# Performance work log

Hardware: AMD Instinct MI355X
Metric: run time of the kernel (lower is better)

Reference implementation:

```python
import jax, jax.numpy as jnp
import numpy as np

N_ATOMS = 100000
N_MOLS = 2500
MAX_NB = 10
HID = 256
ATOM_FDIM = 151
FEAT_DIM = 200
FFN_HID = 1024
N_TASKS = 12
LN_EPS = 1e-5


def setup_inputs() -> dict:
    key = jax.random.key(0)
    ks = jax.random.split(key, 12)
    atoms_per_mol = N_ATOMS // N_MOLS  # 40
    starts = jnp.arange(N_MOLS, dtype=jnp.int32) * atoms_per_mol
    sizes = jnp.full((N_MOLS,), atoms_per_mol, dtype=jnp.int32)
    a_scope = jnp.stack([starts, sizes], axis=1)  # [M, 2]
    d_in = HID + ATOM_FDIM  # 407
    d_ff = 4 * HID          # 1024
    d_mol_in = HID + FEAT_DIM  # 456
    def lin(k, fan_in, shape):
        return jax.random.uniform(k, shape, jnp.float32, -1.0, 1.0) / np.sqrt(fan_in)
    return {
        "atom_output": jax.random.normal(ks[0], (N_ATOMS, HID), jnp.float32),
        "original_f_atoms": jax.random.uniform(ks[1], (N_ATOMS, ATOM_FDIM), jnp.float32),
        "a2a": jax.random.randint(ks[2], (N_ATOMS, MAX_NB), 0, N_ATOMS, jnp.int32),
        "a_scope": a_scope,
        "features_batch": jax.random.normal(ks[3], (N_MOLS, FEAT_DIM), jnp.float32),
        "W1": lin(ks[4], d_in, (d_in, d_ff)), "b1": jnp.zeros((d_ff,), jnp.float32),
        "W2": lin(ks[5], d_ff, (d_ff, HID)), "b2": jnp.zeros((HID,), jnp.float32),
        "ln_g": jnp.ones((HID,), jnp.float32), "ln_b": jnp.zeros((HID,), jnp.float32),
        "Wm1": lin(ks[6], d_mol_in, (d_mol_in, FFN_HID)), "bm1": jnp.zeros((FFN_HID,), jnp.float32),
        "Wm2": lin(ks[7], FFN_HID, (FFN_HID, N_TASKS)), "bm2": jnp.zeros((N_TASKS,), jnp.float32),
    }


def reference(atom_output, original_f_atoms, a2a, a_scope, features_batch,
              W1, b1, W2, b2, ln_g, ln_b, Wm1, bm1, Wm2, bm2):
    # select_neighbor_and_aggregate: gather neighbor embeddings and sum
    aggr = atom_output[a2a].sum(axis=1)                      # [N, HID]
    x = jnp.concatenate([original_f_atoms, aggr], axis=1)    # [N, HID+ATOM_FDIM]
    # PositionwiseFeedForward (dropout = identity at eval)
    h = jax.nn.relu(x @ W1 + b1) @ W2 + b2                   # [N, HID]
    # SublayerConnection with x=None: LayerNorm (dropout identity)
    mu = h.mean(axis=-1, keepdims=True)
    var = ((h - mu) ** 2).mean(axis=-1, keepdims=True)
    h = (h - mu) * jax.lax.rsqrt(var + LN_EPS) * ln_g + ln_b
    # Readout: mean over variable-length a_scope ranges (segment mean)
    starts = a_scope[:, 0]
    sizes = a_scope[:, 1]
    n_mols = a_scope.shape[0]
    seg_ids = jnp.searchsorted(starts, jnp.arange(h.shape[0], dtype=starts.dtype), side="right") - 1
    sums = jax.ops.segment_sum(h, seg_ids, num_segments=n_mols)   # [M, HID]
    mol = sums / sizes[:, None].astype(h.dtype)
    # concat molecule-level features, then mol FFN (2 layers)
    mol = jnp.concatenate([mol, features_batch], axis=1)          # [M, HID+FEAT_DIM]
    out = jax.nn.relu(mol @ Wm1 + bm1) @ Wm2 + bm2                # [M, N_TASKS]
    return out
```

## Files before the change

### kernel.cpp

```cpp
#include <hip/hip_runtime.h>

typedef __attribute__((ext_vector_type(8))) short bfrag;
typedef __attribute__((ext_vector_type(4))) float f32x4;

__device__ __forceinline__ float bf2f(unsigned short u) {
    union { unsigned u32; float f; } cv; cv.u32 = ((unsigned)u) << 16; return cv.f;
}
__device__ __forceinline__ unsigned short f2bf(float f) {
    union { float f; unsigned u; } cv; cv.f = f;
    unsigned u = cv.u;
    unsigned r = (u + 0x7fffu + ((u >> 16) & 1u)) >> 16;
    return (unsigned short)r;
}
__device__ __forceinline__ void gll16(const void* g, void* l) {
    __builtin_amdgcn_global_load_lds(
        (const __attribute__((address_space(1))) unsigned int*)g,
        (__attribute__((address_space(3))) unsigned int*)l, 16, 0, 0);
}

__global__ void to_bf16(const float* __restrict__ src, unsigned short* __restrict__ dst, size_t n) {
    size_t i = ((size_t)blockIdx.x * 256 + threadIdx.x) * 8;
    if (i >= n) return;
    float4 a = *reinterpret_cast<const float4*>(src + i);
    float4 b = *reinterpret_cast<const float4*>(src + i + 4);
    ushort4 o0 = {f2bf(a.x), f2bf(a.y), f2bf(a.z), f2bf(a.w)};
    ushort4 o1 = {f2bf(b.x), f2bf(b.y), f2bf(b.z), f2bf(b.w)};
    *reinterpret_cast<ushort4*>(dst + i) = o0;
    *reinterpret_cast<ushort4*>(dst + i + 4) = o1;
}

__global__ void transpose_pad(const float* __restrict__ W, unsigned short* __restrict__ WT,
                              int R, int Cn, int Kp, int split, int shiftA, int split2, int shiftB) {
    __shared__ unsigned short tile[32][33];
    int r0 = blockIdx.x * 32, c0 = blockIdx.y * 32;
#pragma unroll
    for (int j = 0; j < 4; j++) {
        int r = r0 + threadIdx.y + j * 8;
        int c = c0 + threadIdx.x;
        float v = (r < R) ? W[(size_t)r * Cn + c] : 0.f;
        tile[threadIdx.y + j * 8][threadIdx.x] = f2bf(v);
    }
    __syncthreads();
#pragma unroll
    for (int j = 0; j < 4; j++) {
        int c = c0 + threadIdx.y + j * 8;
        int r = r0 + threadIdx.x;
        int kn = (r < split) ? r + shiftA : (r < split2 ? r + shiftB : r);
        WT[(size_t)c * Kp + kn] = tile[threadIdx.x][threadIdx.y + j * 8];
    }
}

__global__ __launch_bounds__(256) void gather2(const unsigned short* __restrict__ abf,
                                               const float* __restrict__ f_atoms,
                                               const int* __restrict__ a2a,
                                               unsigned short* __restrict__ xb, int n_real) {
    int r = blockIdx.x * 4 + (threadIdx.x >> 6);
    int lane = threadIdx.x & 63;
    unsigned short* xrow = xb + (size_t)r * 448;
    if (r >= n_real) {
        *reinterpret_cast<ushort4*>(xrow + lane * 4) = ushort4{0, 0, 0, 0};
        if (lane < 48) *reinterpret_cast<ushort4*>(xrow + 256 + lane * 4) = ushort4{0, 0, 0, 0};
        return;
    }
    int v = (lane < 10) ? a2a[(size_t)r * 10 + lane] : 0;
    ushort4 u[10];
#pragma unroll
    for (int j = 0; j < 10; j++) {
        int nbj = __shfl(v, j);
        u[j] = *reinterpret_cast<const ushort4*>(abf + (size_t)nbj * 256 + lane * 4);
    }
    float a0 = 0.f, a1 = 0.f, a2 = 0.f, a3 = 0.f;
#pragma unroll
    for (int j = 0; j < 10; j++) {
        a0 += bf2f(u[j].x);
        a1 += bf2f(u[j].y);
        a2 += bf2f(u[j].z);
        a3 += bf2f(u[j].w);
    }
    ushort4 o = {f2bf(a0), f2bf(a1), f2bf(a2), f2bf(a3)};
    *reinterpret_cast<ushort4*>(xrow + lane * 4) = o;
    const float* fr = f_atoms + (size_t)r * 151;
#pragma unroll
    for (int s = 0; s < 3; s++) {
        int c = lane + s * 64;
        if (c < 151) xrow[256 + c] = f2bf(fr[c]);
    }
    if (lane < 41) xrow[407 + lane] = 0;
}

template <int RELU>
__global__ __launch_bounds__(256) void gemm_bt(const unsigned short* __restrict__ A,
                                               const unsigned short* __restrict__ BT,
                                               const float* __restrict__ bias,
                                               unsigned short* __restrict__ C,
                                               int NB, int N, int K) {
    __shared__ __align__(16) unsigned short As[128 * 64];
    __shared__ __align__(16) unsigned short Bs[128 * 64];
    const int t = threadIdx.x;
    const int lane = t & 63, w = t >> 6;
    const int wr = w >> 1, wc = w & 1;

    const int nwg = gridDim.x;
    const int orig = blockIdx.x;
    const int q = nwg >> 3, r8 = nwg & 7;
    const int xcd = orig & 7, slot = orig >> 3;
    const int wgid = (xcd < r8 ? xcd * (q + 1) : r8 * (q + 1) + (xcd - r8) * q) + slot;
    const int bm = (wgid / NB) * 128, bn = (wgid % NB) * 128;

    f32x4 acc[4][4] = {};

    const unsigned short* Ag = A + (size_t)(bm + (t >> 3)) * K + (t & 7) * 8;
    const unsigned short* Bg = BT + (size_t)(bn + (t >> 3)) * K + (t & 7) * 8;
    unsigned short* Al = &As[t * 8];
    unsigned short* Bl = &Bs[t * 8];

    const int la = lane & 15, lb = (lane >> 4) * 8;

    for (int k0 = 0; k0 < K; k0 += 64) {
        __syncthreads();
#pragma unroll
        for (int p = 0; p < 4; p++) gll16(Ag + (size_t)(p * 32) * K + k0, Al + p * 2048);
#pragma unroll
        for (int p = 0; p < 4; p++) gll16(Bg + (size_t)(p * 32) * K + k0, Bl + p * 2048);
        asm volatile("s_waitcnt vmcnt(0)" ::: "memory");
        __syncthreads();
#pragma unroll
        for (int kk = 0; kk < 2; kk++) {
            bfrag a[4], b[4];
#pragma unroll
            for (int i = 0; i < 4; i++)
                a[i] = *reinterpret_cast<const bfrag*>(&As[(wr * 64 + i * 16 + la) * 64 + kk * 32 + lb]);
#pragma unroll
            for (int i = 0; i < 4; i++)
                b[i] = *reinterpret_cast<const bfrag*>(&Bs[(wc * 64 + i * 16 + la) * 64 + kk * 32 + lb]);
#pragma unroll
            for (int i = 0; i < 4; i++)
#pragma unroll
                for (int j = 0; j < 4; j++)
                    acc[i][j] = __builtin_amdgcn_mfma_f32_16x16x32_bf16(a[i], b[j], acc[i][j], 0, 0, 0);
        }
    }

#pragma unroll
    for (int j = 0; j < 4; j++) {
        int col = bn + wc * 64 + j * 16 + la;
        float bv = bias[col];
#pragma unroll
        for (int i = 0; i < 4; i++) {
            int rbase = bm + wr * 64 + i * 16 + (lane >> 4) * 4;
#pragma unroll
            for (int r = 0; r < 4; r++) {
                float v = acc[i][j][r] + bv;
                if (RELU) v = fmaxf(v, 0.f);
                C[(size_t)(rbase + r) * N + col] = f2bf(v);
            }
        }
    }
}

__global__ __launch_bounds__(512) void seg_ln_mean(const unsigned short* __restrict__ h,
                                                   const int* __restrict__ a_scope,
                                                   const float* __restrict__ g,
                                                   const float* __restrict__ b,
                                                   const float* __restrict__ feats,
                                                   unsigned short* __restrict__ mol, int n_mols) {
    __shared__ float part[8][256];
    int m = blockIdx.x, t = threadIdx.x;
    unsigned short* mrow = mol + (size_t)m * 512;
    if (m >= n_mols) {
        mrow[t] = 0;
        return;
    }
    int w = t >> 6, lane = t & 63;
    int start = a_scope[2 * m], size = a_scope[2 * m + 1];
    float4 gv = *reinterpret_cast<const float4*>(g + lane * 4);
    float4 bv = *reinterpret_cast<const float4*>(b + lane * 4);
    float a0 = 0.f, a1 = 0.f, a2 = 0.f, a3 = 0.f;
    for (int r = w; r < size; r += 8) {
        const unsigned short* hp = h + (size_t)(start + r) * 256 + lane * 4;
        ushort4 u = *reinterpret_cast<const ushort4*>(hp);
        float v0 = bf2f(u.x), v1 = bf2f(u.y), v2 = bf2f(u.z), v3 = bf2f(u.w);
        float s = v0 + v1 + v2 + v3;
        float q2 = v0 * v0 + v1 * v1 + v2 * v2 + v3 * v3;
#pragma unroll
        for (int off = 32; off; off >>= 1) {
            s += __shfl_xor(s, off);
            q2 += __shfl_xor(q2, off);
        }
        float mean = s * (1.f / 256.f);
        float var = q2 * (1.f / 256.f) - mean * mean;
        float rs = rsqrtf(var + 1e-5f);
        a0 += (v0 - mean) * rs * gv.x + bv.x;
        a1 += (v1 - mean) * rs * gv.y + bv.y;
        a2 += (v2 - mean) * rs * gv.z + bv.z;
        a3 += (v3 - mean) * rs * gv.w + bv.w;
    }
    part[w][lane * 4 + 0] = a0;
    part[w][lane * 4 + 1] = a1;
    part[w][lane * 4 + 2] = a2;
    part[w][lane * 4 + 3] = a3;
    __syncthreads();
    if (t < 256) {
        float sum = 0.f;
#pragma unroll
        for (int i = 0; i < 8; i++) sum += part[i][t];
        mrow[t] = f2bf(sum / (float)size);
    } else {
        int c = t - 256;
        float fv = (c < 200) ? feats[(size_t)m * 200 + c] : 0.f;
        mrow[256 + c] = f2bf(fv);
    }
}

__global__ void ffn2(const unsigned short* __restrict__ m1, const float* __restrict__ Wm2,
                     const float* __restrict__ bm2, float* __restrict__ out, int n_mols) {
    int wid = blockIdx.x * 4 + (threadIdx.x >> 6);
    if (wid >= n_mols) return;
    int lane = threadIdx.x & 63;
    float acc[12] = {};
    const unsigned short* row = m1 + (size_t)wid * 1024;
#pragma unroll 4
    for (int i = 0; i < 16; i++) {
        int k = i * 64 + lane;
        float v = bf2f(row[k]);
        const float* wr_ = Wm2 + (size_t)k * 12;
#pragma unroll
        for (int tsk = 0; tsk < 12; tsk++) acc[tsk] += v * wr_[tsk];
    }
#pragma unroll
    for (int tsk = 0; tsk < 12; tsk++) {
        float sv = acc[tsk];
#pragma unroll
        for (int off = 32; off; off >>= 1) sv += __shfl_xor(sv, off);
        if (lane == 0) out[(size_t)wid * 12 + tsk] = sv + bm2[tsk];
    }
}

extern "C" void kernel_launch(void* const* d_in, const int* in_sizes, int n_in,
                              void* d_out, int out_size, void* d_ws, size_t ws_size,
                              hipStream_t stream) {
    const float* atom_output = (const float*)d_in[0];
    const float* f_atoms     = (const float*)d_in[1];
    const int*   a2a         = (const int*)d_in[2];
    const int*   a_scope     = (const int*)d_in[3];
    const float* feats       = (const float*)d_in[4];
    const float* W1  = (const float*)d_in[5];
    const float* b1  = (const float*)d_in[6];
    const float* W2  = (const float*)d_in[7];
    const float* b2  = (const float*)d_in[8];
    const float* ln_g = (const float*)d_in[9];
    const float* ln_b = (const float*)d_in[10];
    const float* Wm1 = (const float*)d_in[11];
    const float* bm1 = (const float*)d_in[12];
    const float* Wm2 = (const float*)d_in[13];
    const float* bm2 = (const float*)d_in[14];
    float* out = (float*)d_out;

    char* ws = (char*)d_ws;
    size_t off = 0;
    auto alloc = [&](size_t bytes) {
        void* p = ws + off;
        off += (bytes + 255) & ~(size_t)255;
        return p;
    };
    unsigned short* h     = (unsigned short*)alloc((size_t)100096 * 256 * 2);
    unsigned short* h1    = (unsigned short*)alloc((size_t)50048 * 1024 * 2);
    unsigned short* xf    = (unsigned short*)alloc((size_t)100096 * 448 * 2);
    unsigned short* abf   = (unsigned short*)alloc((size_t)100000 * 256 * 2);
    unsigned short* mol   = (unsigned short*)alloc((size_t)2560 * 512 * 2);
    unsigned short* m1b   = (unsigned short*)alloc((size_t)2560 * 1024 * 2);
    unsigned short* W1bT  = (unsigned short*)alloc((size_t)1024 * 448 * 2);
    unsigned short* W2bT  = (unsigned short*)alloc((size_t)256 * 1024 * 2);
    unsigned short* Wm1bT = (unsigned short*)alloc((size_t)1024 * 512 * 2);

    transpose_pad<<<dim3(14, 32), dim3(32, 8), 0, stream>>>(W1, W1bT, 407, 1024, 448, 151, 256, 407, -151);
    transpose_pad<<<dim3(32, 8),  dim3(32, 8), 0, stream>>>(W2, W2bT, 1024, 256, 1024, 0, 0, 0, 0);
    transpose_pad<<<dim3(16, 32), dim3(32, 8), 0, stream>>>(Wm1, Wm1bT, 456, 1024, 512, 0, 0, 0, 0);

    to_bf16<<<12500, 256, 0, stream>>>(atom_output, abf, (size_t)100000 * 256);
    gather2<<<25024, 256, 0, stream>>>(abf, f_atoms, a2a, xf, 100000);

    for (int c = 0; c < 2; c++) {
        int row0 = c * 50048;
        gemm_bt<1><<<391 * 8, 256, 0, stream>>>(xf + (size_t)row0 * 448, W1bT, b1, h1, 8, 1024, 448);
        gemm_bt<0><<<391 * 2, 256, 0, stream>>>(h1, W2bT, b2, h + (size_t)row0 * 256, 2, 256, 1024);
    }

    seg_ln_mean<<<2560, 512, 0, stream>>>(h, a_scope, ln_g, ln_b, feats, mol, 2500);
    gemm_bt<1><<<160, 256, 0, stream>>>(mol, Wm1bT, bm1, m1b, 8, 1024, 512);
    ffn2<<<625, 256, 0, stream>>>(m1b, Wm2, bm2, out, 2500);
}
```

Baseline: 467.8 us.

## Double-buffer GEMM LDS tiles and XOR-swizzle to avoid bank conflicts

The GEMM kernel now keeps two LDS buffers per operand and prefetches the next K tile with global_load_lds while computing on the current one, waiting only for the older batch of loads. The global source columns are XOR-swizzled by row so that the MFMA fragment reads from LDS spread across banks instead of conflicting. This doubles LDS use per block to 64KB, which may lower occupancy, and relies on the vmcnt(8) count matching the eight loads issued per stage.

```diff
diff --git a/kernel.cpp b/kernel.cpp
--- a/kernel.cpp
+++ b/kernel.cpp
@@ -94,8 +94,8 @@
                                                const float* __restrict__ bias,
                                                unsigned short* __restrict__ C,
                                                int NB, int N, int K) {
-    __shared__ __align__(16) unsigned short As[128 * 64];
-    __shared__ __align__(16) unsigned short Bs[128 * 64];
+    __shared__ __align__(16) unsigned short As[2][128 * 64];
+    __shared__ __align__(16) unsigned short Bs[2][128 * 64];
     const int t = threadIdx.x;
     const int lane = t & 63, w = t >> 6;
     const int wr = w >> 1, wc = w & 1;
@@ -109,36 +109,55 @@
 
     f32x4 acc[4][4] = {};
 
-    const unsigned short* Ag = A + (size_t)(bm + (t >> 3)) * K + (t & 7) * 8;
-    const unsigned short* Bg = BT + (size_t)(bn + (t >> 3)) * K + (t & 7) * 8;
-    unsigned short* Al = &As[t * 8];
-    unsigned short* Bl = &Bs[t * 8];
-
-    const int la = lane & 15, lb = (lane >> 4) * 8;
-
+    const int trow = t >> 3;
+    const int tsl8 = (((t & 7) ^ (trow & 7))) * 8;
+    const unsigned short* Ag = A + (size_t)(bm + trow) * K + tsl8;
+    const unsigned short* Bg = BT + (size_t)(bn + trow) * K + tsl8;
+
+    const int la = lane & 15, hi = lane >> 4;
+
+    auto stage = [&](int buf, int kk0) {
+#pragma unroll
+        for (int p = 0; p < 4; p++) gll16(Ag + (size_t)(p * 32) * K + kk0, &As[buf][t * 8 + p * 2048]);
+#pragma unroll
+        for (int p = 0; p < 4; p++) gll16(Bg + (size_t)(p * 32) * K + kk0, &Bs[buf][t * 8 + p * 2048]);
+    };
+
+    stage(0, 0);
+    int cur = 0;
     for (int k0 = 0; k0 < K; k0 += 64) {
-        __syncthreads();
-#pragma unroll
-        for (int p = 0; p < 4; p++) gll16(Ag + (size_t)(p * 32) * K + k0, Al + p * 2048);
-#pragma unroll
-        for (int p = 0; p < 4; p++) gll16(Bg + (size_t)(p * 32) * K + k0, Bl + p * 2048);
-        asm volatile("s_waitcnt vmcnt(0)" ::: "memory");
-        __syncthreads();
+        __builtin_amdgcn_s_barrier();
+        if (k0 + 64 < K) {
+            stage(cur ^ 1, k0 + 64);
+            asm volatile("s_waitcnt vmcnt(8)" ::: "memory");
+        } else {
+            asm volatile("s_waitcnt vmcnt(0)" ::: "memory");
+        }
+        __builtin_amdgcn_s_barrier();
+
+        const unsigned short* Ab = &As[cur][0];
+        const unsigned short* Bb = &Bs[cur][0];
 #pragma unroll
         for (int kk = 0; kk < 2; kk++) {
+            const int sl = kk * 4 + hi;
             bfrag a[4], b[4];
 #pragma unroll
-            for (int i = 0; i < 4; i++)
-                a[i] = *reinterpret_cast<const bfrag*>(&As[(wr * 64 + i * 16 + la) * 64 + kk * 32 + lb]);
-#pragma unroll
-            for (int i = 0; i < 4; i++)
-                b[i] = *reinterpret_cast<const bfrag*>(&Bs[(wc * 64 + i * 16 + la) * 64 + kk * 32 + lb]);
+            for (int i = 0; i < 4; i++) {
+                int row = wr * 64 + i * 16 + la;
+                a[i] = *reinterpret_cast<const bfrag*>(&Ab[row * 64 + ((sl ^ (la & 7)) * 8)]);
+            }
+#pragma unroll
+            for (int i = 0; i < 4; i++) {
+                int row = wc * 64 + i * 16 + la;
+                b[i] = *reinterpret_cast<const bfrag*>(&Bb[row * 64 + ((sl ^ (la & 7)) * 8)]);
+            }
 #pragma unroll
             for (int i = 0; i < 4; i++)
 #pragma unroll
                 for (int j = 0; j < 4; j++)
                     acc[i][j] = __builtin_amdgcn_mfma_f32_16x16x32_bf16(a[i], b[j], acc[i][j], 0, 0, 0);
         }
+        cur ^= 1;
     }
 
 #pragma unroll
@@ -147,7 +166,7 @@
         float bv = bias[col];
 #pragma unroll
         for (int i = 0; i < 4; i++) {
-            int rbase = bm + wr * 64 + i * 16 + (lane >> 4) * 4;
+            int rbase = bm + wr * 64 + i * 16 + hi * 4;
 #pragma unroll
             for (int r = 0; r < 4; r++) {
                 float v = acc[i][j][r] + bv;
```

Result: faster. 426.5 us (-8.8%).

## Replace 128x128 GEMM with double-buffered swizzled 256x256 tile kernel

Applied to the files above, without the earlier changes.

Replaces the single-buffered 128x128 tile GEMM with a 512-thread 256x256 tile kernel. It double-buffers LDS, prefetches the next K tile in quadrant stages between MFMA phases, XOR-swizzles the LDS layout to avoid bank conflicts, and raises wave priority around the MFMA blocks. The two-chunk FFN loop is merged into one full-size pass by enlarging h1, which also aliases the bf16 atom buffer. The aim is more data reuse per tile and overlap of loads with compute, in exchange for more LDS and register pressure and far fewer blocks for the small N=256 and mol GEMMs.

```diff
diff --git a/kernel.cpp b/kernel.cpp
--- a/kernel.cpp
+++ b/kernel.cpp
@@ -17,6 +17,8 @@
         (const __attribute__((address_space(1))) unsigned int*)g,
         (__attribute__((address_space(3))) unsigned int*)l, 16, 0, 0);
 }
+#define SB  __builtin_amdgcn_sched_barrier(0)
+#define BAR __builtin_amdgcn_s_barrier()
 
 __global__ void to_bf16(const float* __restrict__ src, unsigned short* __restrict__ dst, size_t n) {
     size_t i = ((size_t)blockIdx.x * 256 + threadIdx.x) * 8;
@@ -89,73 +91,144 @@
 }
 
 template <int RELU>
-__global__ __launch_bounds__(256) void gemm_bt(const unsigned short* __restrict__ A,
-                                               const unsigned short* __restrict__ BT,
-                                               const float* __restrict__ bias,
-                                               unsigned short* __restrict__ C,
-                                               int NB, int N, int K) {
-    __shared__ __align__(16) unsigned short As[128 * 64];
-    __shared__ __align__(16) unsigned short Bs[128 * 64];
+__global__ __launch_bounds__(512, 2) void gemm256(const unsigned short* __restrict__ A,
+                                                  const unsigned short* __restrict__ BT,
+                                                  const float* __restrict__ bias,
+                                                  unsigned short* __restrict__ C,
+                                                  int NB, int N, int K) {
+    __shared__ __align__(16) unsigned short As[2][16384];
+    __shared__ __align__(16) unsigned short Bs[2][16384];
     const int t = threadIdx.x;
-    const int lane = t & 63, w = t >> 6;
-    const int wr = w >> 1, wc = w & 1;
-
-    const int nwg = gridDim.x;
-    const int orig = blockIdx.x;
+    const int lane = t & 63, wid = t >> 6;
+    const int wr = wid >> 2, wc = wid & 3;
+    const int la = lane & 15, hi = lane >> 4;
+
+    const int nwg = gridDim.x, orig = blockIdx.x;
     const int q = nwg >> 3, r8 = nwg & 7;
     const int xcd = orig & 7, slot = orig >> 3;
     const int wgid = (xcd < r8 ? xcd * (q + 1) : r8 * (q + 1) + (xcd - r8) * q) + slot;
-    const int bm = (wgid / NB) * 128, bn = (wgid % NB) * 128;
-
-    f32x4 acc[4][4] = {};
-
-    const unsigned short* Ag = A + (size_t)(bm + (t >> 3)) * K + (t & 7) * 8;
-    const unsigned short* Bg = BT + (size_t)(bn + (t >> 3)) * K + (t & 7) * 8;
-    unsigned short* Al = &As[t * 8];
-    unsigned short* Bl = &Bs[t * 8];
-
-    const int la = lane & 15, lb = (lane >> 4) * 8;
-
-    for (int k0 = 0; k0 < K; k0 += 64) {
-        __syncthreads();
-#pragma unroll
-        for (int p = 0; p < 4; p++) gll16(Ag + (size_t)(p * 32) * K + k0, Al + p * 2048);
-#pragma unroll
-        for (int p = 0; p < 4; p++) gll16(Bg + (size_t)(p * 32) * K + k0, Bl + p * 2048);
-        asm volatile("s_waitcnt vmcnt(0)" ::: "memory");
-        __syncthreads();
-#pragma unroll
-        for (int kk = 0; kk < 2; kk++) {
-            bfrag a[4], b[4];
-#pragma unroll
-            for (int i = 0; i < 4; i++)
-                a[i] = *reinterpret_cast<const bfrag*>(&As[(wr * 64 + i * 16 + la) * 64 + kk * 32 + lb]);
-#pragma unroll
-            for (int i = 0; i < 4; i++)
-                b[i] = *reinterpret_cast<const bfrag*>(&Bs[(wc * 64 + i * 16 + la) * 64 + kk * 32 + lb]);
-#pragma unroll
-            for (int i = 0; i < 4; i++)
-#pragma unroll
-                for (int j = 0; j < 4; j++)
-                    acc[i][j] = __builtin_amdgcn_mfma_f32_16x16x32_bf16(a[i], b[j], acc[i][j], 0, 0, 0);
-        }
-    }
-
-#pragma unroll
-    for (int j = 0; j < 4; j++) {
-        int col = bn + wc * 64 + j * 16 + la;
-        float bv = bias[col];
+    const int bm = (wgid / NB) * 256, bn = (wgid % NB) * 256;
+
+    const int trow = t >> 3, tslot = t & 7;
+    const int tsrc = (tslot ^ (trow & 7)) * 8;
+    const unsigned short* Ag = A + (size_t)(bm + trow) * K + tsrc;
+    const unsigned short* Bg = BT + (size_t)(bn + trow) * K + tsrc;
+    const int ldst = trow * 64 + tslot * 8;
+
+    const int NT = K >> 6;
+
+    auto stageA = [&](int buf, int h, int kt) {
+        gll16(Ag + ((size_t)(h * 128) * K + kt * 64), &As[buf][h * 8192 + ldst]);
+        gll16(Ag + ((size_t)(h * 128 + 64) * K + kt * 64), &As[buf][h * 8192 + 4096 + ldst]);
+    };
+    auto stageB = [&](int buf, int h, int kt) {
+        gll16(Bg + ((size_t)(h * 128) * K + kt * 64), &Bs[buf][h * 8192 + ldst]);
+        gll16(Bg + ((size_t)(h * 128 + 64) * K + kt * 64), &Bs[buf][h * 8192 + 4096 + ldst]);
+    };
+    auto rdA = [&](const unsigned short* Ab, int mh, int kk, bfrag* a) {
 #pragma unroll
         for (int i = 0; i < 4; i++) {
-            int rbase = bm + wr * 64 + i * 16 + (lane >> 4) * 4;
-#pragma unroll
-            for (int r = 0; r < 4; r++) {
-                float v = acc[i][j][r] + bv;
-                if (RELU) v = fmaxf(v, 0.f);
-                C[(size_t)(rbase + r) * N + col] = f2bf(v);
-            }
-        }
-    }
+            int row = wr * 64 + mh * 128 + i * 16 + la;
+            a[i] = *reinterpret_cast<const bfrag*>(&Ab[row * 64 + (((kk * 4 + hi) ^ (la & 7)) * 8)]);
+        }
+    };
+    auto rdB = [&](const unsigned short* Bb, int nh, int kk, bfrag* b) {
+#pragma unroll
+        for (int j = 0; j < 2; j++) {
+            int row = wc * 32 + nh * 128 + j * 16 + la;
+            b[j] = *reinterpret_cast<const bfrag*>(&Bb[row * 64 + (((kk * 4 + hi) ^ (la & 7)) * 8)]);
+        }
+    };
+
+    f32x4 acc[8][4] = {};
+
+#define MFMA_Q(mh, nh)                                                                              \
+    _Pragma("unroll") for (int i = 0; i < 4; i++) {                                                 \
+        _Pragma("unroll") for (int j = 0; j < 2; j++) {                                             \
+            acc[(mh)*4 + i][(nh)*2 + j] =                                                           \
+                __builtin_amdgcn_mfma_f32_16x16x32_bf16(a0[i], b0[j], acc[(mh)*4 + i][(nh)*2 + j],  \
+                                                        0, 0, 0);                                   \
+            acc[(mh)*4 + i][(nh)*2 + j] =                                                           \
+                __builtin_amdgcn_mfma_f32_16x16x32_bf16(a1[i], b1[j], acc[(mh)*4 + i][(nh)*2 + j],  \
+                                                        0, 0, 0);                                   \
+        }                                                                                           \
+    }
+
+    stageA(0, 0, 0); stageB(0, 0, 0); stageA(0, 1, 0); stageB(0, 1, 0);
+    if (NT > 1) stageA(1, 0, 1);
+    SB;
+    if (NT > 1) asm volatile("s_waitcnt vmcnt(2)" ::: "memory");
+    else        asm volatile("s_waitcnt vmcnt(0)" ::: "memory");
+    SB; BAR; SB;
+
+    int cur = 0;
+    for (int kt = 0; kt < NT; kt++) {
+        const unsigned short* Ab = &As[cur][0];
+        const unsigned short* Bb = &Bs[cur][0];
+        const int nxt = cur ^ 1;
+        bfrag a0[4], a1[4], b0[2], b1[2];
+
+        rdA(Ab, 0, 0, a0); rdA(Ab, 0, 1, a1);
+        rdB(Bb, 0, 0, b0); rdB(Bb, 0, 1, b1);
+        if (kt + 1 < NT) stageB(nxt, 0, kt + 1);
+        SB; BAR; SB;
+        __builtin_amdgcn_s_setprio(1);
+        MFMA_Q(0, 0);
+        __builtin_amdgcn_s_setprio(0);
+        SB; BAR; SB;
+
+        rdB(Bb, 1, 0, b0); rdB(Bb, 1, 1, b1);
+        if (kt + 1 < NT) { stageA(nxt, 1, kt + 1); stageB(nxt, 1, kt + 1); }
+        SB; BAR; SB;
+        __builtin_amdgcn_s_setprio(1);
+        MFMA_Q(0, 1);
+        __builtin_amdgcn_s_setprio(0);
+        SB; BAR; SB;
+
+        rdA(Ab, 1, 0, a0); rdA(Ab, 1, 1, a1);
+        rdB(Bb, 0, 0, b0); rdB(Bb, 0, 1, b1);
+        SB; BAR; SB;
+        __builtin_amdgcn_s_setprio(1);
+        MFMA_Q(1, 0);
+        __builtin_amdgcn_s_setprio(0);
+        SB; BAR; SB;
+
+        rdB(Bb, 1, 0, b0); rdB(Bb, 1, 1, b1);
+        if (kt + 2 < NT) stageA(cur, 0, kt + 2);
+        SB; BAR; SB;
+        __builtin_amdgcn_s_setprio(1);
+        MFMA_Q(1, 1);
+        __builtin_amdgcn_s_setprio(0);
+        SB;
+        if (kt + 1 < NT) {
+            if (kt + 2 < NT) asm volatile("s_waitcnt vmcnt(2)" ::: "memory");
+            else             asm volatile("s_waitcnt vmcnt(0)" ::: "memory");
+        }
+        SB; BAR; SB;
+        cur = nxt;
+    }
+#undef MFMA_Q
+
+#pragma unroll
+    for (int mh = 0; mh < 2; mh++)
+#pragma unroll
+        for (int i = 0; i < 4; i++) {
+            int rbase = bm + wr * 64 + mh * 128 + i * 16 + hi * 4;
+#pragma unroll
+            for (int nh = 0; nh < 2; nh++)
+#pragma unroll
+                for (int j = 0; j < 2; j++) {
+                    int col = bn + wc * 32 + nh * 128 + j * 16 + la;
+                    float bv = bias[col];
+                    f32x4 av = acc[mh * 4 + i][nh * 2 + j];
+#pragma unroll
+                    for (int r = 0; r < 4; r++) {
+                        float v = av[r] + bv;
+                        if (RELU) v = fmaxf(v, 0.f);
+                        C[(size_t)(rbase + r) * N + col] = f2bf(v);
+                    }
+                }
+        }
 }
 
 __global__ __launch_bounds__(512) void seg_ln_mean(const unsigned short* __restrict__ h,
@@ -264,14 +337,14 @@
         return p;
     };
     unsigned short* h     = (unsigned short*)alloc((size_t)100096 * 256 * 2);
-    unsigned short* h1    = (unsigned short*)alloc((size_t)50048 * 1024 * 2);
+    unsigned short* h1    = (unsigned short*)alloc((size_t)100096 * 1024 * 2);
     unsigned short* xf    = (unsigned short*)alloc((size_t)100096 * 448 * 2);
-    unsigned short* abf   = (unsigned short*)alloc((size_t)100000 * 256 * 2);
     unsigned short* mol   = (unsigned short*)alloc((size_t)2560 * 512 * 2);
     unsigned short* m1b   = (unsigned short*)alloc((size_t)2560 * 1024 * 2);
     unsigned short* W1bT  = (unsigned short*)alloc((size_t)1024 * 448 * 2);
     unsigned short* W2bT  = (unsigned short*)alloc((size_t)256 * 1024 * 2);
     unsigned short* Wm1bT = (unsigned short*)alloc((size_t)1024 * 512 * 2);
+    unsigned short* abf   = h1;
 
     transpose_pad<<<dim3(14, 32), dim3(32, 8), 0, stream>>>(W1, W1bT, 407, 1024, 448, 151, 256, 407, -151);
     transpose_pad<<<dim3(32, 8),  dim3(32, 8), 0, stream>>>(W2, W2bT, 1024, 256, 1024, 0, 0, 0, 0);
@@ -280,13 +353,10 @@
     to_bf16<<<12500, 256, 0, stream>>>(atom_output, abf, (size_t)100000 * 256);
     gather2<<<25024, 256, 0, stream>>>(abf, f_atoms, a2a, xf, 100000);
 
-    for (int c = 0; c < 2; c++) {
-        int row0 = c * 50048;
-        gemm_bt<1><<<391 * 8, 256, 0, stream>>>(xf + (size_t)row0 * 448, W1bT, b1, h1, 8, 1024, 448);
-        gemm_bt<0><<<391 * 2, 256, 0, stream>>>(h1, W2bT, b2, h + (size_t)row0 * 256, 2, 256, 1024);
-    }
+    gemm256<1><<<391 * 4, 512, 0, stream>>>(xf, W1bT, b1, h1, 4, 1024, 448);
+    gemm256<0><<<391 * 1, 512, 0, stream>>>(h1, W2bT, b2, h, 1, 256, 1024);
 
     seg_ln_mean<<<2560, 512, 0, stream>>>(h, a_scope, ln_g, ln_b, feats, mol, 2500);
-    gemm_bt<1><<<160, 256, 0, stream>>>(mol, Wm1bT, bm1, m1b, 8, 1024, 512);
+    gemm256<1><<<10 * 4, 512, 0, stream>>>(mol, Wm1bT, bm1, m1b, 4, 1024, 512);
     ffn2<<<625, 256, 0, stream>>>(m1b, Wm2, bm2, out, 2500);
 }
```

Measured after the change: 425.3 us. 1.1x faster.

## Replace GEMM with wider-tile XOR-swizzled kernel and drop row chunking

Applied to the files above, without the earlier changes.

Replaces the 128x128 GEMM with a 512-thread kernel using 128xBN tiles (BN up to 512), so more B reuse per A tile and fewer blocks. LDS layout is XOR-swizzled to avoid bank conflicts. MFMA operands are swapped so each lane holds four consecutive output columns, allowing vectorized bias loads and ushort4 stores. The two-chunk loop over rows becomes a single launch per layer with a full-size h1 buffer, reusing h1 memory for the bf16 atom copy. Larger LDS footprint (80KB for BN=512) and more accumulators may reduce occupancy.

```diff
diff --git a/kernel.cpp b/kernel.cpp
--- a/kernel.cpp
+++ b/kernel.cpp
@@ -88,72 +88,80 @@
     if (lane < 41) xrow[407 + lane] = 0;
 }
 
-template <int RELU>
-__global__ __launch_bounds__(256) void gemm_bt(const unsigned short* __restrict__ A,
-                                               const unsigned short* __restrict__ BT,
-                                               const float* __restrict__ bias,
-                                               unsigned short* __restrict__ C,
-                                               int NB, int N, int K) {
+template <int BN, int RELU>
+__global__ __launch_bounds__(512, 4) void gemm_sb(const unsigned short* __restrict__ A,
+                                                  const unsigned short* __restrict__ BT,
+                                                  const float* __restrict__ bias,
+                                                  unsigned short* __restrict__ C,
+                                                  int NB, int N, int K) {
+    constexpr int WN = BN / 4;
+    constexpr int NJ = WN / 16;
     __shared__ __align__(16) unsigned short As[128 * 64];
-    __shared__ __align__(16) unsigned short Bs[128 * 64];
+    __shared__ __align__(16) unsigned short Bs[BN * 64];
     const int t = threadIdx.x;
-    const int lane = t & 63, w = t >> 6;
-    const int wr = w >> 1, wc = w & 1;
-
-    const int nwg = gridDim.x;
-    const int orig = blockIdx.x;
+    const int lane = t & 63, wid = t >> 6;
+    const int wr = wid >> 2, wc = wid & 3;
+    const int la = lane & 15, hi = lane >> 4;
+
+    const int nwg = gridDim.x, orig = blockIdx.x;
     const int q = nwg >> 3, r8 = nwg & 7;
     const int xcd = orig & 7, slot = orig >> 3;
     const int wgid = (xcd < r8 ? xcd * (q + 1) : r8 * (q + 1) + (xcd - r8) * q) + slot;
-    const int bm = (wgid / NB) * 128, bn = (wgid % NB) * 128;
-
-    f32x4 acc[4][4] = {};
-
-    const unsigned short* Ag = A + (size_t)(bm + (t >> 3)) * K + (t & 7) * 8;
-    const unsigned short* Bg = BT + (size_t)(bn + (t >> 3)) * K + (t & 7) * 8;
-    unsigned short* Al = &As[t * 8];
-    unsigned short* Bl = &Bs[t * 8];
-
-    const int la = lane & 15, lb = (lane >> 4) * 8;
-
-    for (int k0 = 0; k0 < K; k0 += 64) {
-        __syncthreads();
-#pragma unroll
-        for (int p = 0; p < 4; p++) gll16(Ag + (size_t)(p * 32) * K + k0, Al + p * 2048);
-#pragma unroll
-        for (int p = 0; p < 4; p++) gll16(Bg + (size_t)(p * 32) * K + k0, Bl + p * 2048);
+    const int bm = (wgid / NB) * 128, bn = (wgid % NB) * BN;
+
+    const int trow = t >> 3, tslot = t & 7;
+    const unsigned short* Ag = A + (size_t)(bm + trow) * K + (tslot ^ (trow & 7)) * 8;
+    const unsigned short* Bg = BT + (size_t)(bn + trow) * K + (tslot ^ (trow & 7)) * 8;
+    const int ldst = trow * 64 + tslot * 8;
+
+    f32x4 acc[4][NJ] = {};
+
+    for (int kt = 0; kt < K; kt += 64) {
+        __builtin_amdgcn_s_barrier();
+#pragma unroll
+        for (int p = 0; p < 2; p++)
+            gll16(Ag + (size_t)(p * 64) * K + kt, &As[p * 4096 + ldst]);
+#pragma unroll
+        for (int p = 0; p < BN / 64; p++)
+            gll16(Bg + (size_t)(p * 64) * K + kt, &Bs[p * 4096 + ldst]);
         asm volatile("s_waitcnt vmcnt(0)" ::: "memory");
-        __syncthreads();
+        __builtin_amdgcn_s_barrier();
 #pragma unroll
         for (int kk = 0; kk < 2; kk++) {
-            bfrag a[4], b[4];
+            bfrag a[4], b[NJ];
+#pragma unroll
+            for (int i = 0; i < 4; i++) {
+                int row = wr * 64 + i * 16 + la;
+                a[i] = *reinterpret_cast<const bfrag*>(&As[row * 64 + (((kk * 4 + hi) ^ (la & 7)) * 8)]);
+            }
+#pragma unroll
+            for (int j = 0; j < NJ; j++) {
+                int row = wc * WN + j * 16 + la;
+                b[j] = *reinterpret_cast<const bfrag*>(&Bs[row * 64 + (((kk * 4 + hi) ^ (la & 7)) * 8)]);
+            }
 #pragma unroll
             for (int i = 0; i < 4; i++)
-                a[i] = *reinterpret_cast<const bfrag*>(&As[(wr * 64 + i * 16 + la) * 64 + kk * 32 + lb]);
-#pragma unroll
-            for (int i = 0; i < 4; i++)
-                b[i] = *reinterpret_cast<const bfrag*>(&Bs[(wc * 64 + i * 16 + la) * 64 + kk * 32 + lb]);
-#pragma unroll
-            for (int i = 0; i < 4; i++)
-#pragma unroll
-                for (int j = 0; j < 4; j++)
-                    acc[i][j] = __builtin_amdgcn_mfma_f32_16x16x32_bf16(a[i], b[j], acc[i][j], 0, 0, 0);
+#pragma unroll
+                for (int j = 0; j < NJ; j++)
+                    acc[i][j] = __builtin_amdgcn_mfma_f32_16x16x32_bf16(b[j], a[i], acc[i][j], 0, 0, 0);
         }
     }
 
 #pragma unroll
-    for (int j = 0; j < 4; j++) {
-        int col = bn + wc * 64 + j * 16 + la;
-        float bv = bias[col];
-#pragma unroll
-        for (int i = 0; i < 4; i++) {
-            int rbase = bm + wr * 64 + i * 16 + (lane >> 4) * 4;
-#pragma unroll
-            for (int r = 0; r < 4; r++) {
-                float v = acc[i][j][r] + bv;
-                if (RELU) v = fmaxf(v, 0.f);
-                C[(size_t)(rbase + r) * N + col] = f2bf(v);
+    for (int i = 0; i < 4; i++) {
+        int row = bm + wr * 64 + i * 16 + la;
+#pragma unroll
+        for (int j = 0; j < NJ; j++) {
+            int col0 = bn + wc * WN + j * 16 + hi * 4;
+            float4 bv = *reinterpret_cast<const float4*>(&bias[col0]);
+            f32x4 av = acc[i][j];
+            float v0 = av[0] + bv.x, v1 = av[1] + bv.y, v2 = av[2] + bv.z, v3 = av[3] + bv.w;
+            if (RELU) {
+                v0 = fmaxf(v0, 0.f); v1 = fmaxf(v1, 0.f);
+                v2 = fmaxf(v2, 0.f); v3 = fmaxf(v3, 0.f);
             }
+            ushort4 o = {f2bf(v0), f2bf(v1), f2bf(v2), f2bf(v3)};
+            *reinterpret_cast<ushort4*>(&C[(size_t)row * N + col0]) = o;
         }
     }
 }
@@ -264,14 +272,14 @@
         return p;
     };
     unsigned short* h     = (unsigned short*)alloc((size_t)100096 * 256 * 2);
-    unsigned short* h1    = (unsigned short*)alloc((size_t)50048 * 1024 * 2);
+    unsigned short* h1    = (unsigned short*)alloc((size_t)100096 * 1024 * 2);
     unsigned short* xf    = (unsigned short*)alloc((size_t)100096 * 448 * 2);
-    unsigned short* abf   = (unsigned short*)alloc((size_t)100000 * 256 * 2);
     unsigned short* mol   = (unsigned short*)alloc((size_t)2560 * 512 * 2);
     unsigned short* m1b   = (unsigned short*)alloc((size_t)2560 * 1024 * 2);
     unsigned short* W1bT  = (unsigned short*)alloc((size_t)1024 * 448 * 2);
     unsigned short* W2bT  = (unsigned short*)alloc((size_t)256 * 1024 * 2);
     unsigned short* Wm1bT = (unsigned short*)alloc((size_t)1024 * 512 * 2);
+    unsigned short* abf   = h1;
 
     transpose_pad<<<dim3(14, 32), dim3(32, 8), 0, stream>>>(W1, W1bT, 407, 1024, 448, 151, 256, 407, -151);
     transpose_pad<<<dim3(32, 8),  dim3(32, 8), 0, stream>>>(W2, W2bT, 1024, 256, 1024, 0, 0, 0, 0);
@@ -280,13 +288,10 @@
     to_bf16<<<12500, 256, 0, stream>>>(atom_output, abf, (size_t)100000 * 256);
     gather2<<<25024, 256, 0, stream>>>(abf, f_atoms, a2a, xf, 100000);
 
-    for (int c = 0; c < 2; c++) {
-        int row0 = c * 50048;
-        gemm_bt<1><<<391 * 8, 256, 0, stream>>>(xf + (size_t)row0 * 448, W1bT, b1, h1, 8, 1024, 448);
-        gemm_bt<0><<<391 * 2, 256, 0, stream>>>(h1, W2bT, b2, h + (size_t)row0 * 256, 2, 256, 1024);
-    }
+    gemm_sb<512, 1><<<782 * 2, 512, 0, stream>>>(xf, W1bT, b1, h1, 2, 1024, 448);
+    gemm_sb<256, 0><<<782, 512, 0, stream>>>(h1, W2bT, b2, h, 1, 256, 1024);
 
     seg_ln_mean<<<2560, 512, 0, stream>>>(h, a_scope, ln_g, ln_b, feats, mol, 2500);
-    gemm_bt<1><<<160, 256, 0, stream>>>(mol, Wm1bT, bm1, m1b, 8, 1024, 512);
+    gemm_sb<512, 1><<<20 * 2, 512, 0, stream>>>(mol, Wm1bT, bm1, m1b, 2, 1024, 512);
     ffn2<<<625, 256, 0, stream>>>(m1b, Wm2, bm2, out, 2500);
 }
```

New measurement: 1.467 ms. +213.7%, slower.
